# Performance work log

Measured on AMD Instinct MI355X. Metric: run time of the kernel, lower is better.

The kernel has to match this reference:

```python
import jax, jax.numpy as jnp
import numpy as np


def _embedding_distances(dictionary, x_flat):
    # dictionary: [D, C], x_flat: [T, C] -> [T, D]
    dict_norms = jnp.sum(dictionary * dictionary, axis=-1)          # [D]
    x_norms = jnp.sum(x_flat * x_flat, axis=-1)                     # [T]
    dots = jnp.einsum('tc,dc->td', x_flat, dictionary)              # [T, D]
    return -2.0 * dots + dict_norms[None, :] + x_norms[:, None]


def _quantize(x, dictionary):
    # x: [N, C, H, W]
    N, C, H, W = x.shape
    cl = jnp.transpose(x, (0, 2, 3, 1))                             # [N, H, W, C]
    diffs = _embedding_distances(dictionary, cl.reshape(-1, C))     # [NHW, D]
    idxs = jnp.argmin(diffs, axis=-1).reshape(N, H, W)              # [N, H, W]
    embedded = jnp.transpose(dictionary[idxs], (0, 3, 1, 2))        # [N, C, H, W]
    embedded_pt = jax.lax.stop_gradient(embedded) + (x - jax.lax.stop_gradient(x))
    return embedded, embedded_pt, idxs


def setup_inputs() -> dict:
    key = jax.random.key(0)
    k1, k2, k3 = jax.random.split(key, 3)
    N, C, H, W, D = 32, 256, 32, 32, 1024
    return {
        'inputs': jax.random.normal(k1, (N, C, H, W), dtype=jnp.float32),
        'inputs_thermal': jax.random.normal(k2, (N, C, H, W), dtype=jnp.float32),
        'dictionary': jax.random.normal(k3, (D, C), dtype=jnp.float32),
    }


def reference(inputs, inputs_thermal, dictionary):
    embedded, embedded_pt, idxs = _quantize(inputs, dictionary)
    embedded_t, embedded_pt_t, idxs_t = _quantize(inputs_thermal, dictionary)
    return (embedded, embedded_pt, idxs, embedded_t, embedded_pt_t, idxs_t)
```

## Files before the change

### kernel.cpp

```cpp
#include <hip/hip_runtime.h>

#define NB    32
#define CCH   256
#define HW    1024
#define NPIX  (NB*HW)
#define DDICT 1024

#define EMB_ELEMS  ((size_t)NB*CCH*HW)
#define SEC_ELEMS  (2*EMB_ELEMS + NPIX)

#define TPX  128
#define TD   128
#define NDT  (DDICT/TD)
#define BK   32
#define NKC  (CCH/BK)
#define NPH  (NDT*NKC)

#define TAU  0.125f

typedef __attribute__((ext_vector_type(8))) short bf16x8;
typedef __attribute__((ext_vector_type(4))) float f32x4;

__device__ inline ushort split_rne(float f, float& rest) {
    uint u = __float_as_uint(f);
    uint r = u + 0x7FFFu + ((u >> 16) & 1u);
    rest = f - __uint_as_float(r & 0xFFFF0000u);
    return (ushort)(r >> 16);
}

__device__ inline ushort rne_bf16(float f) {
    uint u = __float_as_uint(f);
    return (ushort)((u + 0x7FFFu + ((u >> 16) & 1u)) >> 16);
}

__device__ inline void gll16(const void* g, void* l) {
    __builtin_amdgcn_global_load_lds(
        (const __attribute__((address_space(1))) uint*)g,
        (__attribute__((address_space(3))) uint*)l,
        16, 0, 0);
}

__global__ void dict_norms_kernel(const float* __restrict__ dict,
                                  float* __restrict__ norms,
                                  int* __restrict__ cnts) {
    if (blockIdx.x == 0 && threadIdx.x < 2) cnts[threadIdx.x] = 0;
    int d = blockIdx.x * blockDim.x + threadIdx.x;
    if (d < DDICT) {
        const float4* row = (const float4*)(dict + (size_t)d * CCH);
        float s = 0.f;
#pragma unroll 8
        for (int i = 0; i < CCH / 4; ++i) {
            float4 v = row[i];
            s += v.x * v.x + v.y * v.y + v.z * v.z + v.w * v.w;
        }
        norms[d] = s;
    }
}

__global__ void dict_split_kernel(const float* __restrict__ dict,
                                  ushort* __restrict__ dHs,
                                  ushort* __restrict__ dMs,
                                  float* __restrict__ dictT) {
    int d = blockIdx.x;
    int lane = threadIdx.x;
    float4 f = ((const float4*)(dict + (size_t)d * CCH))[lane];
    float v[4] = {f.x, f.y, f.z, f.w};
    ushort h[4], m[4];
#pragma unroll
    for (int i = 0; i < 4; ++i) {
        float r1;
        h[i] = split_rne(v[i], r1);
        m[i] = rne_bf16(r1);
    }
    int c0 = lane * 4;
    int kc = c0 >> 5, oct = (c0 >> 3) & 3, e0 = c0 & 7;
    int dt = d >> 7, dd = d & 127;
    int slot = (oct + (dd >> 1)) & 3;
    size_t base = ((size_t)(dt * NKC + kc)) * 4096 + dd * 32 + slot * 8 + e0;
    *(ushort4*)(dHs + base) = make_ushort4(h[0], h[1], h[2], h[3]);
    *(ushort4*)(dMs + base) = make_ushort4(m[0], m[1], m[2], m[3]);
#pragma unroll
    for (int j = 0; j < 4; ++j)
        dictT[(size_t)(c0 + j) * DDICT + d] = v[j];
}

__global__ __launch_bounds__(256, 2)
void vq_mfma_kernel(const float* __restrict__ x0,
                    const float* __restrict__ x1,
                    const ushort* __restrict__ dHs,
                    const ushort* __restrict__ dMs,
                    const float* __restrict__ norms,
                    const float* __restrict__ dict,
                    float* __restrict__ out,
                    int* __restrict__ cnts,
                    int* __restrict__ lists) {
    __shared__ ushort Bs[3][2][4096];
    __shared__ float nrm_s[DDICT];
    __shared__ int   idx_s[TPX];

    const int t    = threadIdx.x;
    const int lane = t & 63;
    const int wv   = t >> 6;
    const int lx   = lane & 15;
    const int q    = lane >> 4;
    const int m0w  = wv * 32;
    const int z    = blockIdx.y;

    const int g0  = blockIdx.x * TPX;
    const int n   = g0 / HW;
    const int hw0 = g0 % HW;

    const float* x = z ? x1 : x0;
    float* out_base = out + (size_t)z * SEC_ELEMS;
    float* out_idx  = out_base + 2 * EMB_ELEMS;
    int* cnt  = cnts + z;
    int* list = lists + (size_t)z * NPIX;

    *(float4*)(nrm_s + t * 4) = *(const float4*)(norms + t * 4);

    const float* xbase = x + (size_t)n * CCH * HW + hw0 + m0w + lx;
    bf16x8 Ah[8][2], Am[8][2];
#pragma unroll
    for (int kc = 0; kc < NKC; ++kc) {
        float a_f[2][8];
#pragma unroll
        for (int mi = 0; mi < 2; ++mi)
#pragma unroll
            for (int j = 0; j < 8; ++j)
                a_f[mi][j] = xbase[(size_t)(kc * BK + q * 8 + j) * HW + mi * 16];
#pragma unroll
        for (int mi = 0; mi < 2; ++mi)
#pragma unroll
            for (int j = 0; j < 8; ++j) {
                float r1;
                ushort h = split_rne(a_f[mi][j], r1);
                Ah[kc][mi][j] = (short)h;
                Am[kc][mi][j] = (short)rne_bf16(r1);
            }
    }

    auto stage = [&](int p, int b) {
#pragma unroll
        for (int plane = 0; plane < 2; ++plane) {
            const ushort* sp = (plane ? dMs : dHs) + (size_t)p * 4096;
#pragma unroll
            for (int half = 0; half < 2; ++half) {
                gll16(sp + (half * 256 + t) * 8,
                      &Bs[b][plane][half * 2048 + wv * 512]);
            }
        }
    };

    __syncthreads();
    stage(0, 0);
    stage(1, 1);

    float b1r[2][4], b2r[2][4]; int i1r[2][4];
#pragma unroll
    for (int mi = 0; mi < 2; ++mi)
#pragma unroll
        for (int r = 0; r < 4; ++r) {
            b1r[mi][r] = 3.0e38f; b2r[mi][r] = 3.0e38f; i1r[mi][r] = 0;
        }

    int rb = 0;
    int sb = 2;
    for (int dt = 0; dt < NDT; ++dt) {
        f32x4 acc[2][8] = {};
#pragma unroll
        for (int kc = 0; kc < NKC; ++kc) {
            if (dt == NDT - 1 && kc == NKC - 1)
                asm volatile("s_waitcnt vmcnt(0)" ::: "memory");
            else
                asm volatile("s_waitcnt vmcnt(4)" ::: "memory");
            __builtin_amdgcn_s_barrier();
            if (!(dt == NDT - 1 && kc >= NKC - 2))
                stage(dt * 8 + kc + 2, sb);

            const ushort* bb = &Bs[rb][0][0];
            __builtin_amdgcn_s_setprio(1);
#pragma unroll
            for (int ni = 0; ni < 8; ++ni) {
                int nn   = ni * 16 + lx;
                int slot = (q + (nn >> 1)) & 3;
                int off  = nn * 32 + slot * 8;
                bf16x8 Bh = *(const bf16x8*)(bb + off);
                bf16x8 Bm = *(const bf16x8*)(bb + 4096 + off);
#pragma unroll
                for (int mi = 0; mi < 2; ++mi) {
                    f32x4 c = acc[mi][ni];
                    c = __builtin_amdgcn_mfma_f32_16x16x32_bf16(Ah[kc][mi], Bh, c, 0, 0, 0);
                    c = __builtin_amdgcn_mfma_f32_16x16x32_bf16(Ah[kc][mi], Bm, c, 0, 0, 0);
                    c = __builtin_amdgcn_mfma_f32_16x16x32_bf16(Am[kc][mi], Bh, c, 0, 0, 0);
                    acc[mi][ni] = c;
                }
            }
            __builtin_amdgcn_s_setprio(0);
            rb = (rb == 2) ? 0 : rb + 1;
            sb = (sb == 2) ? 0 : sb + 1;
        }

        const int d0 = dt * TD;
        float nrm[8];
#pragma unroll
        for (int ni = 0; ni < 8; ++ni) nrm[ni] = nrm_s[d0 + ni * 16 + lx];

#pragma unroll
        for (int mi = 0; mi < 2; ++mi)
#pragma unroll
            for (int r = 0; r < 4; ++r) {
                float c1 = 3.0e38f, c2 = 3.0e38f; int ci = 0;
#pragma unroll
                for (int ni = 0; ni < 8; ++ni) {
                    float dist = fmaf(-2.f, acc[mi][ni][r], nrm[ni]);
                    if (dist < c1)      { c2 = c1; c1 = dist; ci = ni * 16 + lx; }
                    else if (dist < c2) { c2 = dist; }
                }
#pragma unroll
                for (int off = 1; off < 16; off <<= 1) {
                    float o1 = __shfl_xor(c1, off);
                    int   oi = __shfl_xor(ci, off);
                    float o2 = __shfl_xor(c2, off);
                    if (o1 < c1 || (o1 == c1 && oi < ci)) {
                        c2 = fminf(c1, o2); c1 = o1; ci = oi;
                    } else {
                        c2 = fminf(c2, o1);
                    }
                }
                if (c1 < b1r[mi][r]) {
                    b2r[mi][r] = fminf(b1r[mi][r], c2);
                    b1r[mi][r] = c1;
                    i1r[mi][r] = d0 + ci;
                } else {
                    b2r[mi][r] = fminf(b2r[mi][r], c1);
                }
            }
    }

#pragma unroll
    for (int mi = 0; mi < 2; ++mi)
#pragma unroll
        for (int r = 0; r < 4; ++r) {
            if (lx == 0) {
                int loc = m0w + mi * 16 + q * 4 + r;
                int g = g0 + loc;
                idx_s[loc] = i1r[mi][r];
                out_idx[g] = (float)i1r[mi][r];
                if (b2r[mi][r] - b1r[mi][r] < TAU) {
                    int slot = atomicAdd(cnt, 1);
                    list[slot] = g;
                }
            }
        }
    __syncthreads();

    const int pg = t & 31;
    const int cg = t >> 5;
    const int hwp = hw0 + pg * 4;
    const float* r0 = dict + (size_t)idx_s[pg * 4 + 0] * CCH;
    const float* r1 = dict + (size_t)idx_s[pg * 4 + 1] * CCH;
    const float* r2 = dict + (size_t)idx_s[pg * 4 + 2] * CCH;
    const float* r3 = dict + (size_t)idx_s[pg * 4 + 3] * CCH;
    float* oe = out_base;
    float* op = out_base + EMB_ELEMS;
    const size_t obase = (size_t)n * CCH * HW + hwp;

#pragma unroll
    for (int cq = 0; cq < 8; ++cq) {
        int c = cg * 32 + cq * 4;
        float4 q0 = *(const float4*)(r0 + c);
        float4 q1 = *(const float4*)(r1 + c);
        float4 q2 = *(const float4*)(r2 + c);
        float4 q3 = *(const float4*)(r3 + c);
        float4 v0 = make_float4(q0.x, q1.x, q2.x, q3.x);
        float4 v1 = make_float4(q0.y, q1.y, q2.y, q3.y);
        float4 v2 = make_float4(q0.z, q1.z, q2.z, q3.z);
        float4 v3 = make_float4(q0.w, q1.w, q2.w, q3.w);
        *(float4*)(oe + obase + (size_t)(c + 0) * HW) = v0;
        *(float4*)(op + obase + (size_t)(c + 0) * HW) = v0;
        *(float4*)(oe + obase + (size_t)(c + 1) * HW) = v1;
        *(float4*)(op + obase + (size_t)(c + 1) * HW) = v1;
        *(float4*)(oe + obase + (size_t)(c + 2) * HW) = v2;
        *(float4*)(op + obase + (size_t)(c + 2) * HW) = v2;
        *(float4*)(oe + obase + (size_t)(c + 3) * HW) = v3;
        *(float4*)(op + obase + (size_t)(c + 3) * HW) = v3;
    }
}

__global__ __launch_bounds__(256)
void vq_rescue_kernel(const float* __restrict__ x0,
                      const float* __restrict__ x1,
                      const float* __restrict__ dictT,
                      const float* __restrict__ dict,
                      const float* __restrict__ norms,
                      const int* __restrict__ cnts,
                      const int* __restrict__ lists,
                      float* __restrict__ out) {
    __shared__ float xr[CCH];
    __shared__ float rd_s[4];
    __shared__ int   ri_s[4];
    __shared__ int   bi_s;
    const int z = blockIdx.z;
    const float* x = z ? x1 : x0;
    const int* list = lists + (size_t)z * NPIX;
    float* out_emb    = out + (size_t)z * SEC_ELEMS;
    float* out_emb_pt = out_emb + EMB_ELEMS;
    float* out_idx    = out_emb + 2 * EMB_ELEMS;
    const int t    = threadIdx.x;
    const int lane = t & 63;
    const int wv   = t >> 6;
    const int total = cnts[z];

    for (int w = blockIdx.x; w < total; w += gridDim.x) {
        const int g  = list[w];
        const int n  = g / HW;
        const int hw = g % HW;
        xr[t] = x[(size_t)n * CCH * HW + (size_t)t * HW + hw];
        __syncthreads();

        float bd = 3.0e38f; int bi = 0;
#pragma unroll
        for (int dd = 0; dd < 4; ++dd) {
            int d = dd * 256 + t;
            float dot = 0.f;
#pragma unroll 8
            for (int k = 0; k < CCH; ++k)
                dot = fmaf(xr[k], dictT[(size_t)k * DDICT + d], dot);
            float dist = fmaf(-2.f, dot, norms[d]);
            if (dist < bd) { bd = dist; bi = d; }
        }
#pragma unroll
        for (int off = 1; off < 64; off <<= 1) {
            float od = __shfl_xor(bd, off);
            int   oi = __shfl_xor(bi, off);
            if (od < bd || (od == bd && oi < bi)) { bd = od; bi = oi; }
        }
        if (lane == 0) { rd_s[wv] = bd; ri_s[wv] = bi; }
        __syncthreads();
        if (t == 0) {
            float fb = rd_s[0]; int fi = ri_s[0];
#pragma unroll
            for (int q2 = 1; q2 < 4; ++q2)
                if (rd_s[q2] < fb || (rd_s[q2] == fb && ri_s[q2] < fi)) {
                    fb = rd_s[q2]; fi = ri_s[q2];
                }
            bi_s = fi;
            out_idx[g] = (float)fi;
        }
        __syncthreads();
        float v = dict[(size_t)bi_s * CCH + t];
        size_t o = (size_t)n * CCH * HW + (size_t)t * HW + hw;
        out_emb[o]    = v;
        out_emb_pt[o] = v;
        __syncthreads();
    }
}

extern "C" void kernel_launch(void* const* d_in, const int* in_sizes, int n_in,
                              void* d_out, int out_size, void* d_ws, size_t ws_size,
                              hipStream_t stream) {
    const float* x0   = (const float*)d_in[0];
    const float* x1   = (const float*)d_in[1];
    const float* dict = (const float*)d_in[2];
    float* out = (float*)d_out;

    float*  norms = (float*)d_ws;
    ushort* dHs   = (ushort*)(norms + DDICT);
    ushort* dMs   = dHs + (size_t)DDICT * CCH;
    float*  dictT = (float*)(dMs + (size_t)DDICT * CCH);
    int*    lists = (int*)(dictT + (size_t)DDICT * CCH);
    int*    cnts  = lists + 2 * NPIX;

    dict_norms_kernel<<<dim3(DDICT / 256), dim3(256), 0, stream>>>(dict, norms, cnts);
    dict_split_kernel<<<dim3(DDICT), dim3(64), 0, stream>>>(dict, dHs, dMs, dictT);

    vq_mfma_kernel<<<dim3(NPIX / TPX, 2), dim3(256), 0, stream>>>(
        x0, x1, dHs, dMs, norms, dict, out, cnts, lists);

    vq_rescue_kernel<<<dim3(1024, 1, 2), dim3(256), 0, stream>>>(
        x0, x1, dictT, dict, norms, cnts, lists, out);
}
```

Before: 402.8 us.

## Switch dictionary staging to double-buffered 64-wide K chunks with one barrier per chunk

```diff
diff --git a/kernel.cpp b/kernel.cpp
--- a/kernel.cpp
+++ b/kernel.cpp
@@ -14,7 +14,7 @@
 #define NDT  (DDICT/TD)
 #define BK   32
 #define NKC  (CCH/BK)
-#define NPH  (NDT*NKC)
+#define NPH2 (NDT*NKC/2)
 
 #define TAU  0.125f
 
@@ -94,7 +94,7 @@
                     float* __restrict__ out,
                     int* __restrict__ cnts,
                     int* __restrict__ lists) {
-    __shared__ ushort Bs[3][2][4096];
+    __shared__ ushort Bs[2][2][8192];
     __shared__ float nrm_s[DDICT];
     __shared__ int   idx_s[TPX];
 
@@ -142,18 +142,17 @@
     auto stage = [&](int p, int b) {
 #pragma unroll
         for (int plane = 0; plane < 2; ++plane) {
-            const ushort* sp = (plane ? dMs : dHs) + (size_t)p * 4096;
-#pragma unroll
-            for (int half = 0; half < 2; ++half) {
-                gll16(sp + (half * 256 + t) * 8,
-                      &Bs[b][plane][half * 2048 + wv * 512]);
+            const ushort* sp = (plane ? dMs : dHs) + (size_t)p * 8192;
+#pragma unroll
+            for (int h = 0; h < 4; ++h) {
+                gll16(sp + (h * 256 + t) * 8,
+                      &Bs[b][plane][h * 2048 + wv * 512]);
             }
         }
     };
 
     __syncthreads();
     stage(0, 0);
-    stage(1, 1);
 
     float b1r[2][4], b2r[2][4]; int i1r[2][4];
 #pragma unroll
@@ -163,41 +162,38 @@
             b1r[mi][r] = 3.0e38f; b2r[mi][r] = 3.0e38f; i1r[mi][r] = 0;
         }
 
-    int rb = 0;
-    int sb = 2;
     for (int dt = 0; dt < NDT; ++dt) {
         f32x4 acc[2][8] = {};
 #pragma unroll
-        for (int kc = 0; kc < NKC; ++kc) {
-            if (dt == NDT - 1 && kc == NKC - 1)
-                asm volatile("s_waitcnt vmcnt(0)" ::: "memory");
-            else
-                asm volatile("s_waitcnt vmcnt(4)" ::: "memory");
+        for (int kh = 0; kh < 4; ++kh) {
+            const int p = dt * 4 + kh;
+            asm volatile("s_waitcnt vmcnt(0)" ::: "memory");
             __builtin_amdgcn_s_barrier();
-            if (!(dt == NDT - 1 && kc >= NKC - 2))
-                stage(dt * 8 + kc + 2, sb);
-
-            const ushort* bb = &Bs[rb][0][0];
+            if (p + 1 < NPH2) stage(p + 1, (p + 1) & 1);
+
+            const ushort* bb = &Bs[p & 1][0][0];
             __builtin_amdgcn_s_setprio(1);
 #pragma unroll
             for (int ni = 0; ni < 8; ++ni) {
                 int nn   = ni * 16 + lx;
                 int slot = (q + (nn >> 1)) & 3;
                 int off  = nn * 32 + slot * 8;
-                bf16x8 Bh = *(const bf16x8*)(bb + off);
-                bf16x8 Bm = *(const bf16x8*)(bb + 4096 + off);
-#pragma unroll
-                for (int mi = 0; mi < 2; ++mi) {
-                    f32x4 c = acc[mi][ni];
-                    c = __builtin_amdgcn_mfma_f32_16x16x32_bf16(Ah[kc][mi], Bh, c, 0, 0, 0);
-                    c = __builtin_amdgcn_mfma_f32_16x16x32_bf16(Ah[kc][mi], Bm, c, 0, 0, 0);
-                    c = __builtin_amdgcn_mfma_f32_16x16x32_bf16(Am[kc][mi], Bh, c, 0, 0, 0);
-                    acc[mi][ni] = c;
+#pragma unroll
+                for (int kk = 0; kk < 2; ++kk) {
+                    const int kc = kh * 2 + kk;
+                    bf16x8 Bh = *(const bf16x8*)(bb + kk * 4096 + off);
+                    bf16x8 Bm = *(const bf16x8*)(bb + 8192 + kk * 4096 + off);
+#pragma unroll
+                    for (int mi = 0; mi < 2; ++mi) {
+                        f32x4 c = acc[mi][ni];
+                        c = __builtin_amdgcn_mfma_f32_16x16x32_bf16(Ah[kc][mi], Bh, c, 0, 0, 0);
+                        c = __builtin_amdgcn_mfma_f32_16x16x32_bf16(Ah[kc][mi], Bm, c, 0, 0, 0);
+                        c = __builtin_amdgcn_mfma_f32_16x16x32_bf16(Am[kc][mi], Bh, c, 0, 0, 0);
+                        acc[mi][ni] = c;
+                    }
                 }
             }
             __builtin_amdgcn_s_setprio(0);
-            rb = (rb == 2) ? 0 : rb + 1;
-            sb = (sb == 2) ? 0 : sb + 1;
         }
 
         const int d0 = dt * TD;
```

Result: no change. 395.1 us (-1.9%).

## Double pixel tile to 512-thread blocks sharing dictionary stages, add nontemporal IO

Applied to the files above, without the earlier changes.

```diff
diff --git a/kernel.cpp b/kernel.cpp
--- a/kernel.cpp
+++ b/kernel.cpp
@@ -9,7 +9,7 @@
 #define EMB_ELEMS  ((size_t)NB*CCH*HW)
 #define SEC_ELEMS  (2*EMB_ELEMS + NPIX)
 
-#define TPX  128
+#define TPX  256
 #define TD   128
 #define NDT  (DDICT/TD)
 #define BK   32
@@ -38,6 +38,11 @@
         (const __attribute__((address_space(1))) uint*)g,
         (__attribute__((address_space(3))) uint*)l,
         16, 0, 0);
+}
+
+__device__ inline void nts16(float* p, float a, float b, float c, float d) {
+    f32x4 v = {a, b, c, d};
+    __builtin_nontemporal_store(v, (f32x4*)p);
 }
 
 __global__ void dict_norms_kernel(const float* __restrict__ dict,
@@ -84,7 +89,7 @@
         dictT[(size_t)(c0 + j) * DDICT + d] = v[j];
 }
 
-__global__ __launch_bounds__(256, 2)
+__global__ __launch_bounds__(512, 1)
 void vq_mfma_kernel(const float* __restrict__ x0,
                     const float* __restrict__ x1,
                     const ushort* __restrict__ dHs,
@@ -94,7 +99,7 @@
                     float* __restrict__ out,
                     int* __restrict__ cnts,
                     int* __restrict__ lists) {
-    __shared__ ushort Bs[3][2][4096];
+    __shared__ ushort Bs[2][2][4096];
     __shared__ float nrm_s[DDICT];
     __shared__ int   idx_s[TPX];
 
@@ -116,7 +121,7 @@
     int* cnt  = cnts + z;
     int* list = lists + (size_t)z * NPIX;
 
-    *(float4*)(nrm_s + t * 4) = *(const float4*)(norms + t * 4);
+    *(float2*)(nrm_s + t * 2) = *(const float2*)(norms + t * 2);
 
     const float* xbase = x + (size_t)n * CCH * HW + hw0 + m0w + lx;
     bf16x8 Ah[8][2], Am[8][2];
@@ -127,7 +132,8 @@
         for (int mi = 0; mi < 2; ++mi)
 #pragma unroll
             for (int j = 0; j < 8; ++j)
-                a_f[mi][j] = xbase[(size_t)(kc * BK + q * 8 + j) * HW + mi * 16];
+                a_f[mi][j] = __builtin_nontemporal_load(
+                    xbase + (size_t)(kc * BK + q * 8 + j) * HW + mi * 16);
 #pragma unroll
         for (int mi = 0; mi < 2; ++mi)
 #pragma unroll
@@ -143,17 +149,12 @@
 #pragma unroll
         for (int plane = 0; plane < 2; ++plane) {
             const ushort* sp = (plane ? dMs : dHs) + (size_t)p * 4096;
-#pragma unroll
-            for (int half = 0; half < 2; ++half) {
-                gll16(sp + (half * 256 + t) * 8,
-                      &Bs[b][plane][half * 2048 + wv * 512]);
-            }
+            gll16(sp + t * 8, &Bs[b][plane][wv * 512]);
         }
     };
 
     __syncthreads();
     stage(0, 0);
-    stage(1, 1);
 
     float b1r[2][4], b2r[2][4]; int i1r[2][4];
 #pragma unroll
@@ -163,21 +164,16 @@
             b1r[mi][r] = 3.0e38f; b2r[mi][r] = 3.0e38f; i1r[mi][r] = 0;
         }
 
-    int rb = 0;
-    int sb = 2;
     for (int dt = 0; dt < NDT; ++dt) {
         f32x4 acc[2][8] = {};
 #pragma unroll
         for (int kc = 0; kc < NKC; ++kc) {
-            if (dt == NDT - 1 && kc == NKC - 1)
-                asm volatile("s_waitcnt vmcnt(0)" ::: "memory");
-            else
-                asm volatile("s_waitcnt vmcnt(4)" ::: "memory");
+            const int p = dt * 8 + kc;
+            asm volatile("s_waitcnt vmcnt(0)" ::: "memory");
             __builtin_amdgcn_s_barrier();
-            if (!(dt == NDT - 1 && kc >= NKC - 2))
-                stage(dt * 8 + kc + 2, sb);
-
-            const ushort* bb = &Bs[rb][0][0];
+            if (p + 1 < NPH) stage(p + 1, (p + 1) & 1);
+
+            const ushort* bb = &Bs[p & 1][0][0];
             __builtin_amdgcn_s_setprio(1);
 #pragma unroll
             for (int ni = 0; ni < 8; ++ni) {
@@ -196,8 +192,6 @@
                 }
             }
             __builtin_amdgcn_s_setprio(0);
-            rb = (rb == 2) ? 0 : rb + 1;
-            sb = (sb == 2) ? 0 : sb + 1;
         }
 
         const int d0 = dt * TD;
@@ -254,8 +248,8 @@
         }
     __syncthreads();
 
-    const int pg = t & 31;
-    const int cg = t >> 5;
+    const int pg = t & 63;
+    const int cg = t >> 6;
     const int hwp = hw0 + pg * 4;
     const float* r0 = dict + (size_t)idx_s[pg * 4 + 0] * CCH;
     const float* r1 = dict + (size_t)idx_s[pg * 4 + 1] * CCH;
@@ -272,18 +266,14 @@
         float4 q1 = *(const float4*)(r1 + c);
         float4 q2 = *(const float4*)(r2 + c);
         float4 q3 = *(const float4*)(r3 + c);
-        float4 v0 = make_float4(q0.x, q1.x, q2.x, q3.x);
-        float4 v1 = make_float4(q0.y, q1.y, q2.y, q3.y);
-        float4 v2 = make_float4(q0.z, q1.z, q2.z, q3.z);
-        float4 v3 = make_float4(q0.w, q1.w, q2.w, q3.w);
-        *(float4*)(oe + obase + (size_t)(c + 0) * HW) = v0;
-        *(float4*)(op + obase + (size_t)(c + 0) * HW) = v0;
-        *(float4*)(oe + obase + (size_t)(c + 1) * HW) = v1;
-        *(float4*)(op + obase + (size_t)(c + 1) * HW) = v1;
-        *(float4*)(oe + obase + (size_t)(c + 2) * HW) = v2;
-        *(float4*)(op + obase + (size_t)(c + 2) * HW) = v2;
-        *(float4*)(oe + obase + (size_t)(c + 3) * HW) = v3;
-        *(float4*)(op + obase + (size_t)(c + 3) * HW) = v3;
+        nts16(oe + obase + (size_t)(c + 0) * HW, q0.x, q1.x, q2.x, q3.x);
+        nts16(op + obase + (size_t)(c + 0) * HW, q0.x, q1.x, q2.x, q3.x);
+        nts16(oe + obase + (size_t)(c + 1) * HW, q0.y, q1.y, q2.y, q3.y);
+        nts16(op + obase + (size_t)(c + 1) * HW, q0.y, q1.y, q2.y, q3.y);
+        nts16(oe + obase + (size_t)(c + 2) * HW, q0.z, q1.z, q2.z, q3.z);
+        nts16(op + obase + (size_t)(c + 2) * HW, q0.z, q1.z, q2.z, q3.z);
+        nts16(oe + obase + (size_t)(c + 3) * HW, q0.w, q1.w, q2.w, q3.w);
+        nts16(op + obase + (size_t)(c + 3) * HW, q0.w, q1.w, q2.w, q3.w);
     }
 }
 
@@ -374,7 +364,7 @@
     dict_norms_kernel<<<dim3(DDICT / 256), dim3(256), 0, stream>>>(dict, norms, cnts);
     dict_split_kernel<<<dim3(DDICT), dim3(64), 0, stream>>>(dict, dHs, dMs, dictT);
 
-    vq_mfma_kernel<<<dim3(NPIX / TPX, 2), dim3(256), 0, stream>>>(
+    vq_mfma_kernel<<<dim3(NPIX / TPX, 2), dim3(512), 0, stream>>>(
         x0, x1, dHs, dMs, norms, dict, out, cnts, lists);
 
     vq_rescue_kernel<<<dim3(1024, 1, 2), dim3(256), 0, stream>>>(
```

Result: slower. 430.7 us (+6.9%).
